# Performance work log

Measured on AMD Instinct MI355X. Metric: run time of the kernel, lower is better.

## Reference

```python
import jax, jax.numpy as jnp
import numpy as np

B, T, D, H = 4, 2048, 1024, 16
HD = D // H  # head_dim = 64


def setup_inputs() -> dict:
    key = jax.random.key(0)
    k1, k2, k3 = jax.random.split(key, 3)
    x = jax.random.normal(k1, (B, T, D), dtype=jnp.float32)
    # Linear weights stored [in, out] (transpose of torch's [out, in]); scaled init.
    w_qkv = jax.random.normal(k2, (D, 3 * D), dtype=jnp.float32) / np.sqrt(D)
    b_qkv = jnp.zeros((3 * D,), dtype=jnp.float32)
    w_out = jax.random.normal(k3, (D, D), dtype=jnp.float32) / np.sqrt(D)
    b_out = jnp.zeros((D,), dtype=jnp.float32)
    # Causal mask [1,1,T,T]: 1 where attention allowed (j<=i), 0 elsewhere.
    causal_mask = jnp.tril(jnp.ones((T, T), dtype=jnp.int32))[None, None]
    return {"x": x, "causal_mask": causal_mask, "w_qkv": w_qkv,
            "b_qkv": b_qkv, "w_out": w_out, "b_out": b_out}


def reference(x, causal_mask, w_qkv, b_qkv, w_out, b_out):
    b, t, c = x.shape
    qkv = x @ w_qkv + b_qkv                         # [B,T,3D]
    qkv = qkv.reshape(b, t, 3, H, HD)
    q, k, v = jnp.moveaxis(qkv, 2, 0)               # each [B,T,H,HD]
    q = q.transpose(0, 2, 1, 3)                     # [B,H,T,HD]
    k = k.transpose(0, 2, 1, 3)
    v = v.transpose(0, 2, 1, 3)
    att = jnp.einsum('bhqd,bhkd->bhqk', q, k) / np.sqrt(HD).astype(np.float32)
    att = jnp.where(causal_mask == 0, jnp.float32(-jnp.inf), att)
    att = jax.nn.softmax(att, axis=-1)              # dropout=0.0 (eval)
    y = jnp.einsum('bhqk,bhkd->bhqd', att, v)       # [B,H,T,HD]
    y = y.transpose(0, 2, 1, 3).reshape(b, t, c)    # [B,T,D]
    return y @ w_out + b_out
```

## Files before the change

### kernel.cpp

```cpp
#include <hip/hip_runtime.h>
#include <hip/hip_bf16.h>
#include <stdint.h>

#define BB 4
#define TT 2048
#define DD 1024
#define HH 16
#define HDD 64
#define M1 (BB*TT)
#define N1 (3*DD)
#define KDIM DD

typedef __attribute__((ext_vector_type(8))) short short8;
typedef __attribute__((ext_vector_type(4))) float f32x4;

#if __has_builtin(__builtin_amdgcn_exp2f)
#define EXP2(x) __builtin_amdgcn_exp2f(x)
#else
#define EXP2(x) exp2f(x)
#endif

#define GLOAD_LDS16(gp, lp) \
    __builtin_amdgcn_global_load_lds( \
        (const __attribute__((address_space(1))) void*)(gp), \
        (__attribute__((address_space(3))) void*)(lp), 16, 0, 0)

__device__ __forceinline__ float bf2f(unsigned short u) {
    union { uint32_t u32; float f; } c; c.u32 = ((uint32_t)u) << 16; return c.f;
}
__device__ __forceinline__ unsigned short f2bf(float f) {
    union { float f; uint32_t u32; } c; c.f = f;
    uint32_t u = c.u32;
    return (unsigned short)((u + 0x7FFFu + ((u >> 16) & 1u)) >> 16);
}

template <int CTRL>
__device__ __forceinline__ float dpp_ror(float x) {
    union { float f; int i; } u, r;
    u.f = x;
    r.i = __builtin_amdgcn_update_dpp(u.i, u.i, CTRL, 0xF, 0xF, false);
    return r.f;
}
__device__ __forceinline__ float red_max16(float x) {
    x = fmaxf(x, dpp_ror<0x128>(x));
    x = fmaxf(x, dpp_ror<0x124>(x));
    x = fmaxf(x, dpp_ror<0x122>(x));
    x = fmaxf(x, dpp_ror<0x121>(x));
    return x;
}
__device__ __forceinline__ float red_sum16(float x) {
    x += dpp_ror<0x128>(x);
    x += dpp_ror<0x124>(x);
    x += dpp_ror<0x122>(x);
    x += dpp_ror<0x121>(x);
    return x;
}

__global__ __launch_bounds__(256) void cvt_f32_bf16(
    const float* __restrict__ in, unsigned short* __restrict__ out, int n4)
{
    int i = blockIdx.x * 256 + threadIdx.x;
    if (i >= n4) return;
    float4 v = *(const float4*)&in[(size_t)i * 4];
    ushort4 o;
    o.x = f2bf(v.x); o.y = f2bf(v.y); o.z = f2bf(v.z); o.w = f2bf(v.w);
    *(ushort4*)&out[(size_t)i * 4] = o;
}

__global__ __launch_bounds__(256) void transpose_f32_bf16(
    const float* __restrict__ in, unsigned short* __restrict__ out,
    int R, int C)
{
    __shared__ unsigned short tile[32][33];
    int bx = blockIdx.x;
    int by = blockIdx.y;
    int x = bx*32 + threadIdx.x;
    int y0 = by*32 + threadIdx.y;
    #pragma unroll
    for (int i = 0; i < 32; i += 8)
        tile[threadIdx.y + i][threadIdx.x] = f2bf(in[(size_t)(y0 + i)*C + x]);
    __syncthreads();
    int xo = by*32 + threadIdx.x;
    int yo = bx*32 + threadIdx.y;
    #pragma unroll
    for (int i = 0; i < 32; i += 8)
        out[(size_t)(yo + i)*R + xo] = tile[threadIdx.x][threadIdx.y + i];
}

#define TSTR 132
template <int MODE>
__global__ __launch_bounds__(256) void gemm_bf16_mfma(
    const unsigned short* __restrict__ A, const unsigned short* __restrict__ BT,
    const float* __restrict__ bias, void* __restrict__ Cout, void* __restrict__ Cout2,
    int M, int N, int K)
{
    constexpr int SHSZ = (MODE == 2) ? 128*TSTR : 128*64;
    __shared__ __align__(16) unsigned short Sh[SHSZ];
    unsigned short* As = Sh;
    unsigned short* Bs = Sh + 128*32;
    const int tid  = threadIdx.x;
    const int lane = tid & 63;
    const int wave = tid >> 6;
    const int wm = wave >> 1, wn = wave & 1;
    const int quad = lane >> 4, l16 = lane & 15;
    const int m0 = blockIdx.y * 128, n0 = blockIdx.x * 128;

    f32x4 acc[4][4] = {};

    const int nk = K >> 5;
    for (int kt = 0; kt < nk; ++kt) {
        const int k0 = kt << 5;
        __syncthreads();
        #pragma unroll
        for (int h = 0; h < 2; ++h) {
            int c = tid + h*256;
            int row = c >> 2, seg = c & 3;
            GLOAD_LDS16(&A[(size_t)(m0 + row)*K + k0 + seg*8], &As[row*32 + seg*8]);
            GLOAD_LDS16(&BT[(size_t)(n0 + row)*K + k0 + seg*8], &Bs[row*32 + seg*8]);
        }
        __syncthreads();
        short8 af[4], bf[4];
        #pragma unroll
        for (int mi = 0; mi < 4; ++mi)
            af[mi] = *(short8*)&As[(wm*64 + mi*16 + l16)*32 + quad*8];
        #pragma unroll
        for (int ni = 0; ni < 4; ++ni)
            bf[ni] = *(short8*)&Bs[(wn*64 + ni*16 + l16)*32 + quad*8];
        #pragma unroll
        for (int mi = 0; mi < 4; ++mi)
            #pragma unroll
            for (int ni = 0; ni < 4; ++ni)
                acc[mi][ni] = __builtin_amdgcn_mfma_f32_16x16x32_bf16(
                    af[mi], bf[ni], acc[mi][ni], 0, 0, 0);
    }

    if (MODE == 2 && n0 >= 2048) {
        __syncthreads();
        #pragma unroll
        for (int ni = 0; ni < 4; ++ni) {
            int nl = wn*64 + ni*16 + l16;
            float bv = bias[n0 + nl];
            #pragma unroll
            for (int mi = 0; mi < 4; ++mi) {
                ushort4 pk;
                pk.x = f2bf(acc[mi][ni][0] + bv);
                pk.y = f2bf(acc[mi][ni][1] + bv);
                pk.z = f2bf(acc[mi][ni][2] + bv);
                pk.w = f2bf(acc[mi][ni][3] + bv);
                *(ushort4*)&Sh[nl*TSTR + wm*64 + mi*16 + quad*4] = pk;
            }
        }
        __syncthreads();
        const int bb = m0 >> 11, t0 = m0 & 2047;
        #pragma unroll
        for (int p = 0; p < 8; ++p) {
            int c = tid + p*256;
            int row = c >> 4, ch = c & 15;
            int nv = n0 + row - 2048;
            int hv = nv >> 6, dv = nv & 63;
            *(uint4*)&((unsigned short*)Cout2)[((size_t)((bb*16 + hv)*64 + dv))*2048 + t0 + ch*8] =
                *(uint4*)&Sh[row*TSTR + ch*8];
        }
        return;
    }

    const int cstride = (MODE == 2) ? 2048 : N;
    #pragma unroll
    for (int ni = 0; ni < 4; ++ni) {
        int n = n0 + wn*64 + ni*16 + l16;
        float bv = bias[n];
        #pragma unroll
        for (int mi = 0; mi < 4; ++mi) {
            #pragma unroll
            for (int r = 0; r < 4; ++r) {
                int m = m0 + wm*64 + mi*16 + quad*4 + r;
                float val = acc[mi][ni][r] + bv;
                if (MODE == 1)
                    ((float*)Cout)[(size_t)m*cstride + n] = val;
                else
                    ((unsigned short*)Cout)[(size_t)m*cstride + n] = f2bf(val);
            }
        }
    }
}

#define PST 72
__global__ __launch_bounds__(256, 3) void attn_mfma(
    const unsigned short* __restrict__ QK, const unsigned short* __restrict__ VT,
    unsigned short* __restrict__ Y)
{
    __shared__ __align__(16) unsigned short Sh[16384 + 4*32*PST];

    const int tid  = threadIdx.x;
    const int lane = tid & 63;
    const int wave = tid >> 6;
    const int quad = lane >> 4, l16 = lane & 15;

    const int i = blockIdx.x;
    const int xcd = i & 7, j = i >> 3;
    const int qc = 15 - (j & 15);
    const int bh = xcd + 8*(j >> 4);
    const int b = bh >> 4, h = bh & 15;
    const int q0b = qc * 128;
    const int q0w = q0b + wave*32;
    const size_t qkbase = (size_t)(b*TT) * 2048;
    const size_t vbase  = (size_t)(bh*64) * 2048;
    const int qcol = h*64, kcol = 1024 + h*64;
    const float C2 = 0.18033688011112042f;

    unsigned short* Pw = &Sh[16384 + wave*(32*PST)];

    short8 aq[2][2];
    #pragma unroll
    for (int mt = 0; mt < 2; ++mt)
        #pragma unroll
        for (int kk = 0; kk < 2; ++kk)
            aq[mt][kk] = *(const short8*)&QK[qkbase + (size_t)(q0w + mt*16 + l16)*2048
                                            + qcol + kk*32 + quad*8];

    f32x4 o[2][4] = {};
    float mold[2][4], lsum[2][4];
    #pragma unroll
    for (int mt = 0; mt < 2; ++mt)
        #pragma unroll
        for (int r = 0; r < 4; ++r) { mold[mt][r] = -3.0e38f; lsum[mt][r] = 0.0f; }

    const int nkt = 2*qc + 2;

    auto STAGE = [&](int buf, int kt) {
        const int k0 = kt << 6;
        unsigned short* Kb = &Sh[buf*4096];
        unsigned short* Vb = &Sh[8192 + buf*4096];
        #pragma unroll
        for (int p = 0; p < 2; ++p) {
            int c = p*256 + tid;
            int r = c >> 3;
            int ch = (c & 7) ^ (r & 7);
            GLOAD_LDS16(&QK[qkbase + (size_t)(k0 + r)*2048 + kcol + ch*8], &Kb[c*8]);
        }
        #pragma unroll
        for (int p = 0; p < 2; ++p) {
            int c = p*256 + tid;
            int r = c >> 3;
            int ch = (c & 7) ^ (r & 7);
            GLOAD_LDS16(&VT[vbase + (size_t)r*2048 + k0 + ch*8], &Vb[c*8]);
        }
    };

    STAGE(0, 0);
    asm volatile("s_waitcnt vmcnt(0)" ::: "memory");
    __builtin_amdgcn_s_barrier();

    int cur = 0;
    for (int kt = 0; kt < nkt; ++kt) {
        const int k0 = kt * 64;
        if (kt + 1 < nkt) STAGE(cur ^ 1, kt + 1);

        if (k0 <= q0w + 31) {
            const unsigned short* Kb = &Sh[cur*4096];
            const unsigned short* Vb = &Sh[8192 + cur*4096];

            f32x4 s[2][4];
            #pragma unroll
            for (int nt = 0; nt < 4; ++nt) {
                if (k0 + nt*16 <= q0w + 31) {
                    f32x4 z = {};
                    s[0][nt] = z; s[1][nt] = z;
                    #pragma unroll
                    for (int kk = 0; kk < 2; ++kk) {
                        int r = nt*16 + l16;
                        short8 bk = *(const short8*)&Kb[r*64 + (((kk*4 + quad) ^ (r & 7))*8)];
                        s[0][nt] = __builtin_amdgcn_mfma_f32_16x16x32_bf16(aq[0][kk], bk, s[0][nt], 0, 0, 0);
                        s[1][nt] = __builtin_amdgcn_mfma_f32_16x16x32_bf16(aq[1][kk], bk, s[1][nt], 0, 0, 0);
                    }
                } else {
                    #pragma unroll
                    for (int r = 0; r < 4; ++r) { s[0][nt][r] = -3.0e38f; s[1][nt][r] = -3.0e38f; }
                }
            }

            if (k0 + 63 > q0w) {
                #pragma unroll
                for (int mt = 0; mt < 2; ++mt)
                    #pragma unroll
                    for (int nt = 0; nt < 4; ++nt)
                        #pragma unroll
                        for (int r = 0; r < 4; ++r) {
                            int kg = k0 + nt*16 + l16;
                            int qg = q0w + mt*16 + quad*4 + r;
                            if (kg > qg) s[mt][nt][r] = -3.0e38f;
                        }
            }

            float m2n[2][4], al[2][4];
            #pragma unroll
            for (int mt = 0; mt < 2; ++mt)
                #pragma unroll
                for (int r = 0; r < 4; ++r) {
                    float rm = fmaxf(fmaxf(s[mt][0][r], s[mt][1][r]),
                                     fmaxf(s[mt][2][r], s[mt][3][r]));
                    rm = red_max16(rm);
                    float m2 = fmaxf(mold[mt][r], rm * C2);
                    al[mt][r]  = EXP2(mold[mt][r] - m2);
                    m2n[mt][r] = m2;
                }
            float rs[2][4] = {};
            #pragma unroll
            for (int mt = 0; mt < 2; ++mt)
                #pragma unroll
                for (int nt = 0; nt < 4; ++nt)
                    #pragma unroll
                    for (int r = 0; r < 4; ++r) {
                        float p = EXP2(fmaf(s[mt][nt][r], C2, -m2n[mt][r]));
                        s[mt][nt][r] = p;
                        rs[mt][r] += p;
                    }
            #pragma unroll
            for (int mt = 0; mt < 2; ++mt)
                #pragma unroll
                for (int r = 0; r < 4; ++r) {
                    float t = red_sum16(rs[mt][r]);
                    lsum[mt][r] = lsum[mt][r]*al[mt][r] + t;
                    mold[mt][r] = m2n[mt][r];
                }

            #pragma unroll
            for (int mt = 0; mt < 2; ++mt)
                #pragma unroll
                for (int nt = 0; nt < 4; ++nt)
                    #pragma unroll
                    for (int r = 0; r < 4; ++r) {
                        union { float f; uint32_t u; } c; c.f = s[mt][nt][r];
                        Pw[(mt*16 + quad*4 + r)*PST + nt*16 + l16] =
                            (unsigned short)((c.u + 0x8000u) >> 16);
                    }

            #pragma unroll
            for (int mt = 0; mt < 2; ++mt)
                #pragma unroll
                for (int dt = 0; dt < 4; ++dt)
                    #pragma unroll
                    for (int r = 0; r < 4; ++r)
                        o[mt][dt][r] *= al[mt][r];
            short8 bv[2][4];
            #pragma unroll
            for (int kk = 0; kk < 2; ++kk)
                #pragma unroll
                for (int dt = 0; dt < 4; ++dt) {
                    int r = dt*16 + l16;
                    bv[kk][dt] = *(const short8*)&Vb[r*64 + (((kk*4 + quad) ^ (r & 7))*8)];
                }
            #pragma unroll
            for (int kk = 0; kk < 2; ++kk) {
                short8 ap0 = *(short8*)&Pw[(     l16)*PST + kk*32 + quad*8];
                short8 ap1 = *(short8*)&Pw[(16 + l16)*PST + kk*32 + quad*8];
                #pragma unroll
                for (int dt = 0; dt < 4; ++dt) {
                    o[0][dt] = __builtin_amdgcn_mfma_f32_16x16x32_bf16(ap0, bv[kk][dt], o[0][dt], 0, 0, 0);
                    o[1][dt] = __builtin_amdgcn_mfma_f32_16x16x32_bf16(ap1, bv[kk][dt], o[1][dt], 0, 0, 0);
                }
            }
        }

        asm volatile("s_waitcnt vmcnt(0)" ::: "memory");
        __builtin_amdgcn_s_barrier();
        cur ^= 1;
    }

    #pragma unroll
    for (int mt = 0; mt < 2; ++mt)
        #pragma unroll
        for (int r = 0; r < 4; ++r) {
            float inv = 1.0f / lsum[mt][r];
            int t = q0w + mt*16 + quad*4 + r;
            #pragma unroll
            for (int dt = 0; dt < 4; ++dt)
                Y[((size_t)(b*TT + t))*DD + h*64 + dt*16 + l16] = f2bf(o[mt][dt][r] * inv);
        }
}

extern "C" void kernel_launch(void* const* d_in, const int* in_sizes, int n_in,
                              void* d_out, int out_size, void* d_ws, size_t ws_size,
                              hipStream_t stream)
{
    const float* x    = (const float*)d_in[0];
    const float* wqkv = (const float*)d_in[2];
    const float* bqkv = (const float*)d_in[3];
    const float* wout = (const float*)d_in[4];
    const float* bout = (const float*)d_in[5];
    float* out = (float*)d_out;

    char* ws = (char*)d_ws;
    unsigned short* Xb    = (unsigned short*)ws;
    unsigned short* WqkvT = (unsigned short*)(ws + 16777216);
    unsigned short* WoutT = (unsigned short*)(ws + 23068672);
    unsigned short* QK    = (unsigned short*)(ws + 25165824);
    unsigned short* VTb   = (unsigned short*)(ws + 58720256);
    unsigned short* Ybuf  = (unsigned short*)(ws + 75497472);

    cvt_f32_bf16<<<(M1*KDIM/4 + 255)/256, 256, 0, stream>>>(x, Xb, M1*KDIM/4);
    transpose_f32_bf16<<<dim3(N1/32, KDIM/32), dim3(32, 8), 0, stream>>>(wqkv, WqkvT, KDIM, N1);
    transpose_f32_bf16<<<dim3(DD/32, KDIM/32), dim3(32, 8), 0, stream>>>(wout, WoutT, KDIM, DD);
    gemm_bf16_mfma<2><<<dim3(N1/128, M1/128), 256, 0, stream>>>(Xb, WqkvT, bqkv, QK, VTb, M1, N1, KDIM);
    attn_mfma<<<dim3(1024), 256, 0, stream>>>(QK, VTb, Ybuf);
    gemm_bf16_mfma<1><<<dim3(DD/128, M1/128), 256, 0, stream>>>(Ybuf, WoutT, bout, out, nullptr, M1, DD, KDIM);
}
```

Baseline: 353.6 us.

## Pair complementary causal query chunks per attention block to balance work

Each attention block now processes two query chunks, a and 15-a, one after the other in a single continuous K/V loop of 34 tiles. Every block therefore does the same amount of work, and the grid is halved from 1024 to 512 blocks. This removes the tail imbalance of causal attention and drops the per-chunk launch overhead. The V fragment loads from LDS are also moved earlier so they overlap the softmax. The costs are fewer blocks to spread across CUs and extra Q reloads and output stores in the middle of the loop.

```diff
diff --git a/kernel.cpp b/kernel.cpp
--- a/kernel.cpp
+++ b/kernel.cpp
@@ -198,37 +198,57 @@
 
     const int i = blockIdx.x;
     const int xcd = i & 7, j = i >> 3;
-    const int qc = 15 - (j & 15);
-    const int bh = xcd + 8*(j >> 4);
-    const int b = bh >> 4, h = bh & 15;
-    const int q0b = qc * 128;
-    const int q0w = q0b + wave*32;
+    const int a = j & 7;
+    const int bh = xcd + 8*(j >> 3 >> 0 & 0 ? 0 : (j >> 3));
+    (void)bh;
+    const int u = j >> 3;
+    const int bh2 = xcd + 8*u;
+    const int b = bh2 >> 4, h = bh2 & 15;
     const size_t qkbase = (size_t)(b*TT) * 2048;
-    const size_t vbase  = (size_t)(bh*64) * 2048;
+    const size_t vbase  = (size_t)(bh2*64) * 2048;
     const int qcol = h*64, kcol = 1024 + h*64;
     const float C2 = 0.18033688011112042f;
 
     unsigned short* Pw = &Sh[16384 + wave*(32*PST)];
 
+    const int nk1 = 2*a + 2;
+    const int ntot = 34;
+
     short8 aq[2][2];
-    #pragma unroll
-    for (int mt = 0; mt < 2; ++mt)
-        #pragma unroll
-        for (int kk = 0; kk < 2; ++kk)
-            aq[mt][kk] = *(const short8*)&QK[qkbase + (size_t)(q0w + mt*16 + l16)*2048
-                                            + qcol + kk*32 + quad*8];
-
-    f32x4 o[2][4] = {};
+    f32x4 o[2][4];
     float mold[2][4], lsum[2][4];
-    #pragma unroll
-    for (int mt = 0; mt < 2; ++mt)
-        #pragma unroll
-        for (int r = 0; r < 4; ++r) { mold[mt][r] = -3.0e38f; lsum[mt][r] = 0.0f; }
-
-    const int nkt = 2*qc + 2;
-
-    auto STAGE = [&](int buf, int kt) {
-        const int k0 = kt << 6;
+    int q0w = a*128 + wave*32;
+
+    auto LOADQ = [&]() {
+        #pragma unroll
+        for (int mt = 0; mt < 2; ++mt)
+            #pragma unroll
+            for (int kk = 0; kk < 2; ++kk)
+                aq[mt][kk] = *(const short8*)&QK[qkbase + (size_t)(q0w + mt*16 + l16)*2048
+                                                + qcol + kk*32 + quad*8];
+        #pragma unroll
+        for (int mt = 0; mt < 2; ++mt)
+            #pragma unroll
+            for (int r = 0; r < 4; ++r) { mold[mt][r] = -3.0e38f; lsum[mt][r] = 0.0f; }
+        #pragma unroll
+        for (int mt = 0; mt < 2; ++mt)
+            #pragma unroll
+            for (int dt = 0; dt < 4; ++dt) { f32x4 z = {}; o[mt][dt] = z; }
+    };
+    auto FINALIZE = [&]() {
+        #pragma unroll
+        for (int mt = 0; mt < 2; ++mt)
+            #pragma unroll
+            for (int r = 0; r < 4; ++r) {
+                float inv = 1.0f / lsum[mt][r];
+                int tq = q0w + mt*16 + quad*4 + r;
+                #pragma unroll
+                for (int dt = 0; dt < 4; ++dt)
+                    Y[((size_t)(b*TT + tq))*DD + h*64 + dt*16 + l16] = f2bf(o[mt][dt][r] * inv);
+            }
+    };
+
+    auto STAGE = [&](int buf, int k0) {
         unsigned short* Kb = &Sh[buf*4096];
         unsigned short* Vb = &Sh[8192 + buf*4096];
         #pragma unroll
@@ -247,14 +267,23 @@
         }
     };
 
+    LOADQ();
     STAGE(0, 0);
     asm volatile("s_waitcnt vmcnt(0)" ::: "memory");
     __builtin_amdgcn_s_barrier();
 
     int cur = 0;
-    for (int kt = 0; kt < nkt; ++kt) {
-        const int k0 = kt * 64;
-        if (kt + 1 < nkt) STAGE(cur ^ 1, kt + 1);
+    for (int t = 0; t < ntot; ++t) {
+        const int k0 = ((t < nk1) ? t : t - nk1) * 64;
+        if (t + 1 < ntot) {
+            const int t1 = t + 1;
+            STAGE(cur ^ 1, ((t1 < nk1) ? t1 : t1 - nk1) * 64);
+        }
+        if (t == nk1) {
+            FINALIZE();
+            q0w = (15 - a)*128 + wave*32;
+            LOADQ();
+        }
 
         if (k0 <= q0w + 31) {
             const unsigned short* Kb = &Sh[cur*4096];
@@ -278,6 +307,15 @@
                     for (int r = 0; r < 4; ++r) { s[0][nt][r] = -3.0e38f; s[1][nt][r] = -3.0e38f; }
                 }
             }
+
+            short8 bv[2][4];
+            #pragma unroll
+            for (int kk = 0; kk < 2; ++kk)
+                #pragma unroll
+                for (int dt = 0; dt < 4; ++dt) {
+                    int r = dt*16 + l16;
+                    bv[kk][dt] = *(const short8*)&Vb[r*64 + (((kk*4 + quad) ^ (r & 7))*8)];
+                }
 
             if (k0 + 63 > q0w) {
                 #pragma unroll
@@ -319,8 +357,8 @@
             for (int mt = 0; mt < 2; ++mt)
                 #pragma unroll
                 for (int r = 0; r < 4; ++r) {
-                    float t = red_sum16(rs[mt][r]);
-                    lsum[mt][r] = lsum[mt][r]*al[mt][r] + t;
+                    float tsum = red_sum16(rs[mt][r]);
+                    lsum[mt][r] = lsum[mt][r]*al[mt][r] + tsum;
                     mold[mt][r] = m2n[mt][r];
                 }
 
@@ -342,14 +380,6 @@
                     #pragma unroll
                     for (int r = 0; r < 4; ++r)
                         o[mt][dt][r] *= al[mt][r];
-            short8 bv[2][4];
-            #pragma unroll
-            for (int kk = 0; kk < 2; ++kk)
-                #pragma unroll
-                for (int dt = 0; dt < 4; ++dt) {
-                    int r = dt*16 + l16;
-                    bv[kk][dt] = *(const short8*)&Vb[r*64 + (((kk*4 + quad) ^ (r & 7))*8)];
-                }
             #pragma unroll
             for (int kk = 0; kk < 2; ++kk) {
                 short8 ap0 = *(short8*)&Pw[(     l16)*PST + kk*32 + quad*8];
@@ -367,16 +397,7 @@
         cur ^= 1;
     }
 
-    #pragma unroll
-    for (int mt = 0; mt < 2; ++mt)
-        #pragma unroll
-        for (int r = 0; r < 4; ++r) {
-            float inv = 1.0f / lsum[mt][r];
-            int t = q0w + mt*16 + quad*4 + r;
-            #pragma unroll
-            for (int dt = 0; dt < 4; ++dt)
-                Y[((size_t)(b*TT + t))*DD + h*64 + dt*16 + l16] = f2bf(o[mt][dt][r] * inv);
-        }
+    FINALIZE();
 }
 
 extern "C" void kernel_launch(void* const* d_in, const int* in_sizes, int n_in,
@@ -402,6 +423,6 @@
     transpose_f32_bf16<<<dim3(N1/32, KDIM/32), dim3(32, 8), 0, stream>>>(wqkv, WqkvT, KDIM, N1);
     transpose_f32_bf16<<<dim3(DD/32, KDIM/32), dim3(32, 8), 0, stream>>>(wout, WoutT, KDIM, DD);
     gemm_bf16_mfma<2><<<dim3(N1/128, M1/128), 256, 0, stream>>>(Xb, WqkvT, bqkv, QK, VTb, M1, N1, KDIM);
-    attn_mfma<<<dim3(1024), 256, 0, stream>>>(QK, VTb, Ybuf);
+    attn_mfma<<<dim3(512), 256, 0, stream>>>(QK, VTb, Ybuf);
     gemm_bf16_mfma<1><<<dim3(DD/128, M1/128), 256, 0, stream>>>(Ybuf, WoutT, bout, out, nullptr, M1, DD, KDIM);
 }
```

After: 335.2 us. -5.2%, faster.
